# Kernel optimization log

Hardware: AMD Instinct MI355X
Metric: run time of the kernel (lower is better)

Reference implementation:

```python
import jax, jax.numpy as jnp
import numpy as np

# CUBA-LIF constants (from LavaNetwork.__init__ with beta=0.95)
THRESHOLD = 1.0
CURRENT_DECAY = 1.0   # current[t] = (1-1.0)*current[t-1] + input[t] == input[t]
VOLTAGE_DECAY = 1.0 - 0.95  # = 0.05, so v[t] = 0.95*v[t-1] + cur[t]

N_INPUT, N_HIDDEN, N_OUTPUT = 512, 2048, 4 * 64
B, T = 32, 1024


def setup_inputs() -> dict:
    key = jax.random.key(0)
    kx, k1, k2, k3, k4 = jax.random.split(key, 5)
    x = (jax.random.uniform(kx, (B, N_INPUT, T)) < 0.1).astype(jnp.float32)
    # learned params (Linear with bias); small scale so spiking is reasonable
    w1 = jax.random.normal(k1, (N_HIDDEN, N_INPUT), dtype=jnp.float32) * (1.0 / np.sqrt(N_INPUT))
    b1 = jax.random.normal(k2, (N_HIDDEN,), dtype=jnp.float32) * 0.01
    w2 = jax.random.normal(k3, (N_OUTPUT, N_HIDDEN), dtype=jnp.float32) * (1.0 / np.sqrt(N_HIDDEN))
    b2 = jax.random.normal(k4, (N_OUTPUT,), dtype=jnp.float32) * 0.01
    return {"x": x, "w1": w1, "b1": b1, "w2": w2, "b2": b2}


def _cuba_lif(cur):
    """CUBA neuron with current_decay=1 (current==synaptic input),
    leaky-integrate voltage, fire at threshold, reset voltage to 0.
    cur: (B, N, T) -> spikes (B, N, T)."""
    beta_v = 1.0 - VOLTAGE_DECAY  # 0.95

    def step(v, c_t):
        v = v * beta_v + c_t
        s = (v >= THRESHOLD).astype(v.dtype)
        v = v * (1.0 - s)  # reset-to-zero on spike (Loihi behavior)
        return v, s

    cur_t = jnp.moveaxis(cur, -1, 0)  # (T, B, N)
    v0 = jnp.zeros(cur.shape[:-1], cur.dtype)
    _, spk = jax.lax.scan(step, v0, cur_t)
    return jnp.moveaxis(spk, 0, -1)  # (B, N, T)


def reference(x, w1, b1, w2, b2):
    # layer 1: synapse (einsum 'bit,oi->bot' + bias) -> CUBA neuron
    cur1 = jnp.einsum('bit,oi->bot', x, w1) + b1[None, :, None]
    spk1 = _cuba_lif(cur1)
    # layer 2
    cur2 = jnp.einsum('bit,oi->bot', spk1, w2) + b2[None, :, None]
    spk2 = _cuba_lif(cur2)
    return (spk1, spk2)
```

## Files before the change

kernel.cpp:

```cpp
#include <hip/hip_runtime.h>


typedef int i32x4 __attribute__((ext_vector_type(4)));
typedef _Float16 f16x8 __attribute__((ext_vector_type(8)));
typedef _Float16 f16x4 __attribute__((ext_vector_type(4)));
typedef float f32x4 __attribute__((ext_vector_type(4)));

#define GLDS(g, l) __builtin_amdgcn_global_load_lds( \
    (const __attribute__((address_space(1))) void*)(g), \
    (__attribute__((address_space(3))) void*)(l), 16, 0, 0)

#define INV231 4.656612873077392578125e-10


__global__ __launch_bounds__(256) void prep_w8(const float* __restrict__ A,
                                               signed char* __restrict__ wp,
                                               int M, int K)
{
    long gt = (long)blockIdx.x * 256 + threadIdx.x;
    int kq4 = K >> 2;
    int m = (int)(gt / kq4), kq = (int)(gt % kq4);
    int k0 = kq * 4;
    int kt = k0 >> 6, kin = k0 & 63;
    int cw = ((kin >> 4) ^ (m >> 1)) & 3;
    float4 w = *(const float4*)&A[(long)m * K + k0];
    float wv[4] = {w.x, w.y, w.z, w.w};
    int pack[4] = {0, 0, 0, 0};
#pragma unroll
    for (int e = 0; e < 4; e++) {
        long k64 = (long)rint((double)wv[e] * 2147483648.0);
#pragma unroll
        for (int j = 0; j < 3; j++) {
            long r = ((k64 + 128) & 255) - 128;
            pack[j] |= ((int)r & 255) << (e * 8);
            k64 = (k64 - r) >> 8;
        }
        pack[3] |= ((int)k64 & 255) << (e * 8);
    }
#pragma unroll
    for (int p = 0; p < 4; p++)
        *(int*)&wp[(((long)kt * 4 + p) * M + m) * 64 + cw * 16 + (kin & 15)] = pack[p];
}

__global__ __launch_bounds__(256) void prep_x8(const float* __restrict__ x,
                                               unsigned char* __restrict__ xt)
{
    __shared__ float xs[64][68];
    const int b = blockIdx.z, i0 = blockIdx.y * 64, t0 = blockIdx.x * 64;
    const float* xb = x + ((long)b * 512 + i0) * 1024 + t0;
#pragma unroll
    for (int p = 0; p < 4; p++) {
        int f = threadIdx.x + p * 256;
        int i = f >> 4, t4 = (f & 15) * 4;
        *(float4*)&xs[i][t4] = *(const float4*)&xb[(long)i * 1024 + t4];
    }
    __syncthreads();
    int tt = threadIdx.x >> 2, c = threadIdx.x & 3;
    unsigned char bytes[16];
#pragma unroll
    for (int j = 0; j < 16; j++)
        bytes[j] = (unsigned char)xs[c * 16 + j][tt];
    *(uint4*)&xt[(((long)b * 8 + (i0 >> 6)) * 1024 + t0 + tt) * 64 + c * 16] =
        *(uint4*)bytes;
}

__global__ __launch_bounds__(576, 1) void gemm_lif1(
    const signed char* __restrict__ wp,
    const unsigned char* __restrict__ act,
    const float* __restrict__ bias,
    unsigned* __restrict__ mask_ws)
{
    __shared__ signed char Ws[8][4][64][64];
    __shared__ float cs[2][64][64];

    const int m0 = blockIdx.x * 64, b = blockIdx.y;
    const int tid = threadIdx.x, lane = tid & 63, wave = tid >> 6;
    const int lm = lane & 15, lq = lane >> 4;
    const int fro = ((lq ^ (lm >> 1)) & 3) * 16;
    const int mw = wave & 3;
    const int tw2 = wave >> 2;
    const unsigned char* ab = act + (long)b * 8 * 1024 * 64;

    i32x4 areg[4][2];
    double bv = 0.0;

    if (wave < 8) {
        const int gl_row = lane >> 2, gl_col = (lane & 3) * 16;
#pragma unroll
        for (int j = 0; j < 4; ++j) {
            const int r = wave + 8 * j;
            const int kt = r >> 2, pl = r & 3;
            const signed char* g = wp + ((long)r * 2048 + m0 + gl_row) * 64 + gl_col;
#pragma unroll
            for (int q = 0; q < 4; ++q)
                GLDS(g + q * 16 * 64, &Ws[kt][pl][q * 16][0]);
        }
        bv = (double)bias[m0 + mw * 16 + lm];
#pragma unroll
        for (int f = 0; f < 2; f++)
            areg[0][f] = *(const i32x4*)
                &ab[((long)(tw2 * 32 + f * 16 + lm)) * 64 + lq * 16];
#pragma unroll
        for (int f = 0; f < 2; f++)
            areg[1][f] = *(const i32x4*)
                &ab[((long)1 * 1024 + tw2 * 32 + f * 16 + lm) * 64 + lq * 16];
    }
    __syncthreads();

    double u = 0.0;
    bool sprev = false;

    for (int p = 0; p < 17; ++p) {
        if (wave < 8 && p < 16) {
            i32x4 acc[4][2];
#pragma unroll
            for (int pp = 0; pp < 4; pp++)
#pragma unroll
                for (int f = 0; f < 2; f++) acc[pp][f] = (i32x4)0;

#pragma unroll
            for (int kk = 0; kk < 8; ++kk) {
                {
                    int vn = p * 8 + kk + 2;
                    if (vn > 127) vn = 127;
                    const int pn = vn >> 3, kn = vn & 7;
                    const long tt = (long)pn * 64 + tw2 * 32 + lm;
#pragma unroll
                    for (int f = 0; f < 2; f++)
                        areg[(kk + 2) & 3][f] = *(const i32x4*)
                            &ab[((long)kn * 1024 + tt + f * 16) * 64 + lq * 16];
                }
                __builtin_amdgcn_s_setprio(1);
#pragma unroll
                for (int pl = 0; pl < 4; pl++) {
                    i32x4 w0 = *(const i32x4*)&Ws[kk][pl][mw * 16 + lm][fro];
#pragma unroll
                    for (int f = 0; f < 2; f++)
                        acc[pl][f] = __builtin_amdgcn_mfma_i32_16x16x64_i8(
                            areg[kk & 3][f], w0, acc[pl][f], 0, 0, 0);
                }
                __builtin_amdgcn_s_setprio(0);
            }
#pragma unroll
            for (int tf = 0; tf < 2; tf++)
#pragma unroll
                for (int r = 0; r < 4; r++) {
                    long T = acc[3][tf][r];
                    T = T * 256 + acc[2][tf][r];
                    T = T * 256 + acc[1][tf][r];
                    T = T * 256 + acc[0][tf][r];
                    cs[p & 1][tw2 * 32 + tf * 16 + lq * 4 + r][mw * 16 + lm] =
                        (float)((double)T * INV231 + bv);
                }
        }
        if (wave == 8 && p >= 1) {
            const int pq = p - 1, buf = pq & 1;
            float cvA[32], cvB[32];
#pragma unroll
            for (int j = 0; j < 32; ++j) cvA[j] = cs[buf][j][lane];
#pragma unroll
            for (int j = 0; j < 32; ++j) cvB[j] = cs[buf][32 + j][lane];
            {
                unsigned mword = 0;
#pragma unroll
                for (int j = 0; j < 32; ++j) {
                    double c = (double)cvA[j];
                    double a = 0.95 * u + c;
                    u = sprev ? c : a;
                    bool s = (u >= 1.0);
                    mword |= (s ? 1u : 0u) << j;
                    sprev = s;
                }
                mask_ws[((long)b * 32 + pq * 2 + 0) * 2048 + m0 + lane] = mword;
            }
            {
                unsigned mword = 0;
#pragma unroll
                for (int j = 0; j < 32; ++j) {
                    double c = (double)cvB[j];
                    double a = 0.95 * u + c;
                    u = sprev ? c : a;
                    bool s = (u >= 1.0);
                    mword |= (s ? 1u : 0u) << j;
                    sprev = s;
                }
                mask_ws[((long)b * 32 + pq * 2 + 1) * 2048 + m0 + lane] = mword;
            }
        }
        asm volatile("s_waitcnt lgkmcnt(0)" ::: "memory");
        __builtin_amdgcn_s_barrier();
        __builtin_amdgcn_sched_barrier(0);
    }
}

__global__ __launch_bounds__(256) void expand_both(
    const unsigned* __restrict__ mask_ws,
    unsigned char* __restrict__ spk8,
    float* __restrict__ spk1)
{
    __shared__ unsigned msk[64][33];
    const int b = blockIdx.x, kt = blockIdx.y;
    const int tid = threadIdx.x;
#pragma unroll
    for (int i = 0; i < 8; ++i) {
        int idx = tid + i * 256;
        int tw = idx >> 6, m = idx & 63;
        msk[m][tw] = mask_ws[((long)b * 32 + tw) * 2048 + kt * 64 + m];
    }
    __syncthreads();
    unsigned char* dst = spk8 + ((long)b * 32 + kt) * 1024 * 64;
#pragma unroll
    for (int i = 0; i < 16; ++i) {
        int off = tid + i * 256;
        int t = off >> 2, mq = off & 3;
        int tw = t >> 5, sh = t & 31;
        unsigned w0 = 0, w1 = 0, w2 = 0, w3 = 0;
#pragma unroll
        for (int j = 0; j < 4; ++j) {
            w0 |= ((msk[mq * 16 + j][tw] >> sh) & 1u) << (8 * j);
            w1 |= ((msk[mq * 16 + 4 + j][tw] >> sh) & 1u) << (8 * j);
            w2 |= ((msk[mq * 16 + 8 + j][tw] >> sh) & 1u) << (8 * j);
            w3 |= ((msk[mq * 16 + 12 + j][tw] >> sh) & 1u) << (8 * j);
        }
        *(uint4*)&dst[(long)off * 16] = (uint4){w0, w1, w2, w3};
    }
    const int rr = tid >> 5, l5 = tid & 31;
    const int sh1 = (l5 & 7) * 4;
#pragma unroll
    for (int rep = 0; rep < 8; ++rep) {
        const int row = rr + rep * 8;
        float* d1 = spk1 + ((long)b * 2048 + kt * 64 + row) * 1024;
#pragma unroll
        for (int j = 0; j < 8; j++) {
            const int t = l5 * 4 + j * 128;
            const unsigned w = msk[row][(l5 >> 3) + j * 4];
            float4 o;
            o.x = ((w >> sh1) & 1u) ? 1.f : 0.f;
            o.y = ((w >> (sh1 + 1)) & 1u) ? 1.f : 0.f;
            o.z = ((w >> (sh1 + 2)) & 1u) ? 1.f : 0.f;
            o.w = ((w >> (sh1 + 3)) & 1u) ? 1.f : 0.f;
            *(float4*)&d1[t] = o;
        }
    }
}

template <bool TRANS, int NITER, int CHUNK>
__global__ __launch_bounds__(256, 2) void gemm_i8(
    const signed char* __restrict__ wp,
    const unsigned char* __restrict__ act,
    const float* __restrict__ bias,
    float* __restrict__ C,
    int M)
{
    constexpr int NCHUNK = NITER / CHUNK;
    __shared__ signed char Ws[CHUNK][4][32][64];

    const int b = blockIdx.y;
    const int m0 = blockIdx.z * 32, t0 = blockIdx.x * 256;
    const int tid = threadIdx.x, lane = tid & 63, wave = tid >> 6;
    const int wt = t0 + wave * 64;
    const int lm = lane & 15, lq = lane >> 4;
    const int fro = ((lq ^ (lm >> 1)) & 3) * 16;
    const int gl_row = lane >> 2, gl_col = (lane & 3) * 16;

    const unsigned char* ab = act + (long)b * NITER * 1024 * 64;

    auto stage = [&](int cc) {
#pragma unroll
        for (int j = 0; j < CHUNK; ++j) {
            const int r = wave + 4 * j;
            const int kt = r >> 2, p = r & 3;
            const long kg = ((long)(cc * CHUNK + kt) * 4 + p);
            const signed char* g = wp + (kg * M + m0 + gl_row) * 64 + gl_col;
            GLDS(g, &Ws[kt][p][0][0]);
            GLDS(g + 16 * 64, &Ws[kt][p][16][0]);
        }
    };

    i32x4 acc[4][8];
#pragma unroll
    for (int p = 0; p < 4; p++)
#pragma unroll
        for (int q = 0; q < 8; q++) acc[p][q] = (i32x4)0;

    stage(0);
    i32x4 areg[2][4];
#pragma unroll
    for (int f = 0; f < 4; f++)
        areg[0][f] = *(const i32x4*)&ab[((long)(wt + f * 16 + lm)) * 64 + lq * 16];
    __syncthreads();

    for (int c = 0; c < NCHUNK; ++c) {
#pragma unroll
        for (int kk = 0; kk < CHUNK; ++kk) {
            {
                const int itv = c * CHUNK + kk;
                const long nx = (itv + 1 < NITER) ? itv + 1 : itv;
#pragma unroll
                for (int f = 0; f < 4; f++)
                    areg[(kk + 1) & 1][f] = *(const i32x4*)
                        &ab[(nx * 1024 + wt + f * 16 + lm) * 64 + lq * 16];
            }
#pragma unroll
            for (int p = 0; p < 4; p++) {
                i32x4 w0 = *(const i32x4*)&Ws[kk][p][lm][fro];
                i32x4 w1 = *(const i32x4*)&Ws[kk][p][16 + lm][fro];
                if (TRANS) {
#pragma unroll
                    for (int f = 0; f < 4; f++) {
                        acc[p][f * 2 + 0] = __builtin_amdgcn_mfma_i32_16x16x64_i8(
                            areg[kk & 1][f], w0, acc[p][f * 2 + 0], 0, 0, 0);
                        acc[p][f * 2 + 1] = __builtin_amdgcn_mfma_i32_16x16x64_i8(
                            areg[kk & 1][f], w1, acc[p][f * 2 + 1], 0, 0, 0);
                    }
                } else {
#pragma unroll
                    for (int f = 0; f < 4; f++) {
                        acc[p][0 + f] = __builtin_amdgcn_mfma_i32_16x16x64_i8(
                            w0, areg[kk & 1][f], acc[p][0 + f], 0, 0, 0);
                        acc[p][4 + f] = __builtin_amdgcn_mfma_i32_16x16x64_i8(
                            w1, areg[kk & 1][f], acc[p][4 + f], 0, 0, 0);
                    }
                }
            }
        }
        if (c + 1 < NCHUNK) {
            __syncthreads();
            stage(c + 1);
            __syncthreads();
        }
    }

    if (TRANS) {
        double bv[2];
        bv[0] = (double)bias[m0 + lm];
        bv[1] = (double)bias[m0 + 16 + lm];
        float* Cb = C + (long)b * 1024 * M;
#pragma unroll
        for (int tf = 0; tf < 4; tf++)
#pragma unroll
            for (int r = 0; r < 4; r++) {
                const int trow = wt + tf * 16 + lq * 4 + r;
#pragma unroll
                for (int mf = 0; mf < 2; mf++) {
                    long T = acc[3][tf * 2 + mf][r];
                    T = T * 256 + acc[2][tf * 2 + mf][r];
                    T = T * 256 + acc[1][tf * 2 + mf][r];
                    T = T * 256 + acc[0][tf * 2 + mf][r];
                    Cb[(long)trow * M + m0 + mf * 16 + lm] =
                        (float)((double)T * INV231 + bv[mf]);
                }
            }
    } else {
        float* Cb = C + (long)b * M * 1024;
#pragma unroll
        for (int mf = 0; mf < 2; mf++)
#pragma unroll
            for (int r = 0; r < 4; r++) {
                const int mrow = m0 + mf * 16 + lq * 4 + r;
                const double bv = (double)bias[mrow];
#pragma unroll
                for (int tf = 0; tf < 4; tf++) {
                    long T = acc[3][mf * 4 + tf][r];
                    T = T * 256 + acc[2][mf * 4 + tf][r];
                    T = T * 256 + acc[1][mf * 4 + tf][r];
                    T = T * 256 + acc[0][mf * 4 + tf][r];
                    Cb[(long)mrow * 1024 + wt + tf * 16 + lm] =
                        (float)((double)T * INV231 + bv);
                }
            }
    }
}

template <int RPB>
__global__ __launch_bounds__(256) void lif_lds(float* __restrict__ cur)
{
    __shared__ float cs[RPB][36];
    const long rowbase = (long)blockIdx.x * RPB;
    float* base = cur + rowbase * 1024;
    const int tid = threadIdx.x;
    double v = 0.0;
    const int NV = RPB * 32 / 4;
    for (int tc = 0; tc < 1024; tc += 32) {
        for (int f = tid; f < NV; f += 256) {
            int row = f >> 3, t4 = (f & 7) * 4;
            *(float4*)&cs[row][t4] = *(const float4*)&base[(long)row * 1024 + tc + t4];
        }
        __syncthreads();
        if (tid < RPB) {
            float cv[32];
#pragma unroll
            for (int j = 0; j < 32; j++) cv[j] = cs[tid][j];
#pragma unroll
            for (int j = 0; j < 32; j++) {
                v = 0.95 * v + (double)cv[j];
                bool s = v >= 1.0;
                cs[tid][j] = s ? 1.f : 0.f;
                if (s) v = 0.0;
            }
        }
        __syncthreads();
        for (int f = tid; f < NV; f += 256) {
            int row = f >> 3, t4 = (f & 7) * 4;
            *(float4*)&base[(long)row * 1024 + tc + t4] = *(float4*)&cs[row][t4];
        }
        __syncthreads();
    }
}


__device__ inline void split3(float w, _Float16& q0, _Float16& q1, _Float16& q2) {
    float p0 = rintf(w * 4096.f) * 2.44140625e-4f;
    float r1 = w - p0;
    float p1s = rintf(r1 * 8388608.f) * 2.44140625e-4f;
    float r2 = r1 - p1s * 4.8828125e-4f;
    float p2s = rintf(r2 * 1.7179869184e10f) * 1.220703125e-4f;
    q0 = (_Float16)p0; q1 = (_Float16)p1s; q2 = (_Float16)p2s;
}

__global__ __launch_bounds__(256) void gemm_f16x3_kernel(
    const float* __restrict__ A, const float* __restrict__ Bmat,
    const float* __restrict__ bias, float* __restrict__ C,
    int M, int N, int K, long sB, long sC)
{
    __shared__ _Float16 As[3][128][40];
    __shared__ _Float16 Bsh[128][40];
    const int batch = blockIdx.z;
    const float* Bp = Bmat + (long)batch * sB;
    float* Cp = C + (long)batch * sC;
    const int m0 = blockIdx.y * 128, n0 = blockIdx.x * 128;
    const int tid = threadIdx.x, lane = tid & 63, wave = tid >> 6;
    const int wrow = (wave >> 1) * 64, wcol = (wave & 1) * 64;
    const int lm = lane & 15, lq = lane >> 4;
    const int a_mo = tid >> 3, a_kc = (tid & 7) * 4;
    const int b_kq = tid >> 5, b_nq = tid & 31;

    f32x4 acc[3][4][4];
#pragma unroll
    for (int p = 0; p < 3; p++)
#pragma unroll
        for (int i = 0; i < 4; i++)
#pragma unroll
            for (int j = 0; j < 4; j++) acc[p][i][j] = (f32x4)0.f;

    for (int k0 = 0; k0 < K; k0 += 32) {
#pragma unroll
        for (int i = 0; i < 4; i++) {
            const int m = i * 32 + a_mo;
            float4 w = *(const float4*)&A[(long)(m0 + m) * K + k0 + a_kc];
            _Float16 a0[4], a1[4], a2[4];
            split3(w.x, a0[0], a1[0], a2[0]);
            split3(w.y, a0[1], a1[1], a2[1]);
            split3(w.z, a0[2], a1[2], a2[2]);
            split3(w.w, a0[3], a1[3], a2[3]);
            *(f16x4*)&As[0][m][a_kc] = (f16x4){a0[0], a0[1], a0[2], a0[3]};
            *(f16x4*)&As[1][m][a_kc] = (f16x4){a1[0], a1[1], a1[2], a1[3]};
            *(f16x4*)&As[2][m][a_kc] = (f16x4){a2[0], a2[1], a2[2], a2[3]};
        }
        {
            float4 r0 = *(const float4*)&Bp[(long)(k0 + b_kq * 4 + 0) * N + n0 + b_nq * 4];
            float4 r1 = *(const float4*)&Bp[(long)(k0 + b_kq * 4 + 1) * N + n0 + b_nq * 4];
            float4 r2 = *(const float4*)&Bp[(long)(k0 + b_kq * 4 + 2) * N + n0 + b_nq * 4];
            float4 r3 = *(const float4*)&Bp[(long)(k0 + b_kq * 4 + 3) * N + n0 + b_nq * 4];
            *(f16x4*)&Bsh[b_nq * 4 + 0][b_kq * 4] =
                (f16x4){(_Float16)r0.x, (_Float16)r1.x, (_Float16)r2.x, (_Float16)r3.x};
            *(f16x4*)&Bsh[b_nq * 4 + 1][b_kq * 4] =
                (f16x4){(_Float16)r0.y, (_Float16)r1.y, (_Float16)r2.y, (_Float16)r3.y};
            *(f16x4*)&Bsh[b_nq * 4 + 2][b_kq * 4] =
                (f16x4){(_Float16)r0.z, (_Float16)r1.z, (_Float16)r2.z, (_Float16)r3.z};
            *(f16x4*)&Bsh[b_nq * 4 + 3][b_kq * 4] =
                (f16x4){(_Float16)r0.w, (_Float16)r1.w, (_Float16)r2.w, (_Float16)r3.w};
        }
        __syncthreads();
        f16x8 bf[4];
#pragma unroll
        for (int j = 0; j < 4; j++)
            bf[j] = *(const f16x8*)&Bsh[wcol + j * 16 + lm][lq * 8];
#pragma unroll
        for (int p = 0; p < 3; p++) {
            f16x8 af[4];
#pragma unroll
            for (int i = 0; i < 4; i++)
                af[i] = *(const f16x8*)&As[p][wrow + i * 16 + lm][lq * 8];
#pragma unroll
            for (int i = 0; i < 4; i++)
#pragma unroll
                for (int j = 0; j < 4; j++)
                    acc[p][i][j] = __builtin_amdgcn_mfma_f32_16x16x32_f16(
                        af[i], bf[j], acc[p][i][j], 0, 0, 0);
        }
        __syncthreads();
    }
#pragma unroll
    for (int i = 0; i < 4; i++)
#pragma unroll
        for (int r = 0; r < 4; r++) {
            const int row = m0 + wrow + i * 16 + lq * 4 + r;
            const double bv = (double)bias[row];
#pragma unroll
            for (int j = 0; j < 4; j++) {
                double s = (double)acc[0][i][j][r]
                         + (double)acc[1][i][j][r] * 4.8828125e-4
                         + (double)acc[2][i][j][r] * 4.76837158203125e-7 + bv;
                Cp[(long)row * N + n0 + wcol + j * 16 + lm] = (float)s;
            }
        }
}

__global__ __launch_bounds__(256) void lif_rows(float* __restrict__ data,
                                                long nrows, int T)
{
    long r = (long)blockIdx.x * blockDim.x + threadIdx.x;
    if (r >= nrows) return;
    float* p = data + r * (long)T;
    double v = 0.0;
    for (int t = 0; t < T; t += 4) {
        float4 c = *(float4*)(p + t);
        float4 s;
        v = 0.95 * v + (double)c.x; s.x = (v >= 1.0) ? 1.f : 0.f; if (v >= 1.0) v = 0.0;
        v = 0.95 * v + (double)c.y; s.y = (v >= 1.0) ? 1.f : 0.f; if (v >= 1.0) v = 0.0;
        v = 0.95 * v + (double)c.z; s.z = (v >= 1.0) ? 1.f : 0.f; if (v >= 1.0) v = 0.0;
        v = 0.95 * v + (double)c.w; s.w = (v >= 1.0) ? 1.f : 0.f; if (v >= 1.0) v = 0.0;
        *(float4*)(p + t) = s;
    }
}


extern "C" void kernel_launch(void* const* d_in, const int* in_sizes, int n_in,
                              void* d_out, int out_size, void* d_ws, size_t ws_size,
                              hipStream_t stream)
{
    const float* x  = (const float*)d_in[0];
    const float* w1 = (const float*)d_in[1];
    const float* b1 = (const float*)d_in[2];
    const float* w2 = (const float*)d_in[3];
    const float* b2 = (const float*)d_in[4];

    float* out  = (float*)d_out;
    float* spk1 = out;
    float* spk2 = out + (long)32 * 2048 * 1024;

    const size_t WP1 = 4194304;
    const size_t WP2 = 2097152;
    const size_t X8T = 16777216;
    const size_t SPK = 67108864;
    const size_t MSK = 8388608;
    const size_t NEED = WP1 + WP2 + X8T + SPK + MSK;

    if (ws_size >= NEED) {
        char* ws = (char*)d_ws;
        signed char* wp1 = (signed char*)ws;
        signed char* wp2 = (signed char*)(ws + WP1);
        unsigned char* x8t = (unsigned char*)(ws + WP1 + WP2);
        unsigned char* spk8 = (unsigned char*)(ws + WP1 + WP2 + X8T);
        unsigned* mask_ws = (unsigned*)(ws + WP1 + WP2 + X8T + SPK);

        prep_w8<<<1024, 256, 0, stream>>>(w1, wp1, 2048, 512);
        prep_w8<<<512, 256, 0, stream>>>(w2, wp2, 256, 2048);
        prep_x8<<<dim3(16, 8, 32), 256, 0, stream>>>(x, x8t);

        gemm_lif1<<<dim3(32, 32), 576, 0, stream>>>(wp1, x8t, b1, mask_ws);

        expand_both<<<dim3(32, 32), 256, 0, stream>>>(mask_ws, spk8, spk1);

        gemm_i8<false, 32, 8><<<dim3(4, 32, 8), 256, 0, stream>>>(
            wp2, spk8, b2, spk2, 256);
        lif_lds<32><<<256, 256, 0, stream>>>(spk2);
    } else {
        gemm_f16x3_kernel<<<dim3(8, 16, 32), 256, 0, stream>>>(
            w1, x, b1, spk1, 2048, 1024, 512, (long)512 * 1024, (long)2048 * 1024);
        lif_rows<<<(65536 + 255) / 256, 256, 0, stream>>>(spk1, 65536, 1024);
        gemm_f16x3_kernel<<<dim3(8, 2, 32), 256, 0, stream>>>(
            w2, spk1, b2, spk2, 256, 1024, 2048, (long)2048 * 1024, (long)256 * 1024);
        lif_rows<<<(8192 + 255) / 256, 256, 0, stream>>>(spk2, 8192, 1024);
    }
}
```

Baseline: 630.3 us.

## Fuse layer-2 int8 GEMM with LIF scan using producer/consumer waves

Replaces the separate layer-2 int8 GEMM and LDS-based LIF kernel with one kernel. Four waves compute 128-timestep tiles of currents into a double-buffered LDS tile while a fifth wave runs the sequential LIF recurrence on the previous tile and writes spikes directly. This removes the float current round trip through global memory and one kernel launch. In exchange, grid parallelism drops to 512 blocks of 16 rows each at one block per CU, and the serial LIF wave may become the bottleneck.

```diff
diff --git a/kernel.cpp b/kernel.cpp
--- a/kernel.cpp
+++ b/kernel.cpp
@@ -244,167 +244,157 @@
     }
 }
 
-template <bool TRANS, int NITER, int CHUNK>
-__global__ __launch_bounds__(256, 2) void gemm_i8(
+__global__ __launch_bounds__(320, 1) void gemm_lif2(
     const signed char* __restrict__ wp,
     const unsigned char* __restrict__ act,
     const float* __restrict__ bias,
-    float* __restrict__ C,
-    int M)
-{
-    constexpr int NCHUNK = NITER / CHUNK;
-    __shared__ signed char Ws[CHUNK][4][32][64];
-
-    const int b = blockIdx.y;
-    const int m0 = blockIdx.z * 32, t0 = blockIdx.x * 256;
+    float* __restrict__ spk2)
+{
+    __shared__ signed char Ws[32][4][16][64];
+    __shared__ float cs[2][128][17];
+
+    const int b = blockIdx.x, m0 = blockIdx.y * 16;
     const int tid = threadIdx.x, lane = tid & 63, wave = tid >> 6;
-    const int wt = t0 + wave * 64;
     const int lm = lane & 15, lq = lane >> 4;
     const int fro = ((lq ^ (lm >> 1)) & 3) * 16;
-    const int gl_row = lane >> 2, gl_col = (lane & 3) * 16;
-
-    const unsigned char* ab = act + (long)b * NITER * 1024 * 64;
-
-    auto stage = [&](int cc) {
-#pragma unroll
-        for (int j = 0; j < CHUNK; ++j) {
+    const unsigned char* ab = act + (long)b * 32 * 1024 * 64;
+
+    i32x4 areg[4][2];
+    double bvr[4] = {0.0, 0.0, 0.0, 0.0};
+
+    if (wave < 4) {
+        const int gl_row = lane >> 2, gl_col = (lane & 3) * 16;
+#pragma unroll
+        for (int j = 0; j < 32; ++j) {
             const int r = wave + 4 * j;
-            const int kt = r >> 2, p = r & 3;
-            const long kg = ((long)(cc * CHUNK + kt) * 4 + p);
-            const signed char* g = wp + (kg * M + m0 + gl_row) * 64 + gl_col;
-            GLDS(g, &Ws[kt][p][0][0]);
-            GLDS(g + 16 * 64, &Ws[kt][p][16][0]);
-        }
-    };
-
-    i32x4 acc[4][8];
-#pragma unroll
-    for (int p = 0; p < 4; p++)
-#pragma unroll
-        for (int q = 0; q < 8; q++) acc[p][q] = (i32x4)0;
-
-    stage(0);
-    i32x4 areg[2][4];
-#pragma unroll
-    for (int f = 0; f < 4; f++)
-        areg[0][f] = *(const i32x4*)&ab[((long)(wt + f * 16 + lm)) * 64 + lq * 16];
+            const int kt = r >> 2, pl = r & 3;
+            const signed char* g =
+                wp + (((long)kt * 4 + pl) * 256 + m0 + gl_row) * 64 + gl_col;
+            GLDS(g, &Ws[kt][pl][0][0]);
+        }
+#pragma unroll
+        for (int r = 0; r < 4; ++r)
+            bvr[r] = (double)bias[m0 + lq * 4 + r];
+        {
+            const long wt0 = wave * 32 + lm;
+#pragma unroll
+            for (int f = 0; f < 2; f++)
+                areg[0][f] = *(const i32x4*)&ab[(wt0 + f * 16) * 64 + lq * 16];
+#pragma unroll
+            for (int f = 0; f < 2; f++)
+                areg[1][f] = *(const i32x4*)
+                    &ab[((long)1 * 1024 + wt0 + f * 16) * 64 + lq * 16];
+        }
+    }
     __syncthreads();
 
-    for (int c = 0; c < NCHUNK; ++c) {
-#pragma unroll
-        for (int kk = 0; kk < CHUNK; ++kk) {
+    double u = 0.0;
+    bool sprev = false;
+    float* sp2 = spk2 + ((long)b * 256 + m0 + (lane & 15)) * 1024;
+
+    for (int p = 0; p < 9; ++p) {
+        if (wave < 4 && p < 8) {
+            i32x4 acc[4][2];
+#pragma unroll
+            for (int pp = 0; pp < 4; pp++)
+#pragma unroll
+                for (int f = 0; f < 2; f++) acc[pp][f] = (i32x4)0;
+
+#pragma unroll 4
+            for (int kt = 0; kt < 32; ++kt) {
+                {
+                    int vn = p * 32 + kt + 2;
+                    if (vn > 255) vn = 255;
+                    const int pn = vn >> 5, kn = vn & 31;
+                    const long tt = (long)pn * 128 + wave * 32 + lm;
+#pragma unroll
+                    for (int f = 0; f < 2; f++)
+                        areg[(kt + 2) & 3][f] = *(const i32x4*)
+                            &ab[((long)kn * 1024 + tt + f * 16) * 64 + lq * 16];
+                }
+                __builtin_amdgcn_s_setprio(1);
+#pragma unroll
+                for (int pl = 0; pl < 4; pl++) {
+                    i32x4 w0 = *(const i32x4*)&Ws[kt][pl][lm][fro];
+#pragma unroll
+                    for (int f = 0; f < 2; f++)
+                        acc[pl][f] = __builtin_amdgcn_mfma_i32_16x16x64_i8(
+                            w0, areg[kt & 3][f], acc[pl][f], 0, 0, 0);
+                }
+                __builtin_amdgcn_s_setprio(0);
+            }
+#pragma unroll
+            for (int tf = 0; tf < 2; tf++)
+#pragma unroll
+                for (int r = 0; r < 4; r++) {
+                    long T = acc[3][tf][r];
+                    T = T * 256 + acc[2][tf][r];
+                    T = T * 256 + acc[1][tf][r];
+                    T = T * 256 + acc[0][tf][r];
+                    cs[p & 1][wave * 32 + tf * 16 + lm][lq * 4 + r] =
+                        (float)((double)T * INV231 + bvr[r]);
+                }
+        }
+        if (wave == 4 && p >= 1 && lane < 16) {
+            const int pq = p - 1, buf = pq & 1;
+            float* sp = sp2 + pq * 128;
+            float cvA[32], cvB[32];
+#pragma unroll
+            for (int j = 0; j < 32; ++j) cvA[j] = cs[buf][j][lane];
+#pragma unroll
+            for (int j = 0; j < 32; ++j) cvB[j] = cs[buf][32 + j][lane];
             {
-                const int itv = c * CHUNK + kk;
-                const long nx = (itv + 1 < NITER) ? itv + 1 : itv;
-#pragma unroll
-                for (int f = 0; f < 4; f++)
-                    areg[(kk + 1) & 1][f] = *(const i32x4*)
-                        &ab[(nx * 1024 + wt + f * 16 + lm) * 64 + lq * 16];
-            }
-#pragma unroll
-            for (int p = 0; p < 4; p++) {
-                i32x4 w0 = *(const i32x4*)&Ws[kk][p][lm][fro];
-                i32x4 w1 = *(const i32x4*)&Ws[kk][p][16 + lm][fro];
-                if (TRANS) {
-#pragma unroll
-                    for (int f = 0; f < 4; f++) {
-                        acc[p][f * 2 + 0] = __builtin_amdgcn_mfma_i32_16x16x64_i8(
-                            areg[kk & 1][f], w0, acc[p][f * 2 + 0], 0, 0, 0);
-                        acc[p][f * 2 + 1] = __builtin_amdgcn_mfma_i32_16x16x64_i8(
-                            areg[kk & 1][f], w1, acc[p][f * 2 + 1], 0, 0, 0);
-                    }
-                } else {
-#pragma unroll
-                    for (int f = 0; f < 4; f++) {
-                        acc[p][0 + f] = __builtin_amdgcn_mfma_i32_16x16x64_i8(
-                            w0, areg[kk & 1][f], acc[p][0 + f], 0, 0, 0);
-                        acc[p][4 + f] = __builtin_amdgcn_mfma_i32_16x16x64_i8(
-                            w1, areg[kk & 1][f], acc[p][4 + f], 0, 0, 0);
-                    }
-                }
-            }
-        }
-        if (c + 1 < NCHUNK) {
-            __syncthreads();
-            stage(c + 1);
-            __syncthreads();
-        }
-    }
-
-    if (TRANS) {
-        double bv[2];
-        bv[0] = (double)bias[m0 + lm];
-        bv[1] = (double)bias[m0 + 16 + lm];
-        float* Cb = C + (long)b * 1024 * M;
-#pragma unroll
-        for (int tf = 0; tf < 4; tf++)
-#pragma unroll
-            for (int r = 0; r < 4; r++) {
-                const int trow = wt + tf * 16 + lq * 4 + r;
-#pragma unroll
-                for (int mf = 0; mf < 2; mf++) {
-                    long T = acc[3][tf * 2 + mf][r];
-                    T = T * 256 + acc[2][tf * 2 + mf][r];
-                    T = T * 256 + acc[1][tf * 2 + mf][r];
-                    T = T * 256 + acc[0][tf * 2 + mf][r];
-                    Cb[(long)trow * M + m0 + mf * 16 + lm] =
-                        (float)((double)T * INV231 + bv[mf]);
-                }
-            }
-    } else {
-        float* Cb = C + (long)b * M * 1024;
-#pragma unroll
-        for (int mf = 0; mf < 2; mf++)
-#pragma unroll
-            for (int r = 0; r < 4; r++) {
-                const int mrow = m0 + mf * 16 + lq * 4 + r;
-                const double bv = (double)bias[mrow];
-#pragma unroll
-                for (int tf = 0; tf < 4; tf++) {
-                    long T = acc[3][mf * 4 + tf][r];
-                    T = T * 256 + acc[2][mf * 4 + tf][r];
-                    T = T * 256 + acc[1][mf * 4 + tf][r];
-                    T = T * 256 + acc[0][mf * 4 + tf][r];
-                    Cb[(long)mrow * 1024 + wt + tf * 16 + lm] =
-                        (float)((double)T * INV231 + bv);
-                }
-            }
-    }
-}
-
-template <int RPB>
-__global__ __launch_bounds__(256) void lif_lds(float* __restrict__ cur)
-{
-    __shared__ float cs[RPB][36];
-    const long rowbase = (long)blockIdx.x * RPB;
-    float* base = cur + rowbase * 1024;
-    const int tid = threadIdx.x;
-    double v = 0.0;
-    const int NV = RPB * 32 / 4;
-    for (int tc = 0; tc < 1024; tc += 32) {
-        for (int f = tid; f < NV; f += 256) {
-            int row = f >> 3, t4 = (f & 7) * 4;
-            *(float4*)&cs[row][t4] = *(const float4*)&base[(long)row * 1024 + tc + t4];
-        }
-        __syncthreads();
-        if (tid < RPB) {
-            float cv[32];
-#pragma unroll
-            for (int j = 0; j < 32; j++) cv[j] = cs[tid][j];
-#pragma unroll
-            for (int j = 0; j < 32; j++) {
-                v = 0.95 * v + (double)cv[j];
-                bool s = v >= 1.0;
-                cs[tid][j] = s ? 1.f : 0.f;
-                if (s) v = 0.0;
-            }
-        }
-        __syncthreads();
-        for (int f = tid; f < NV; f += 256) {
-            int row = f >> 3, t4 = (f & 7) * 4;
-            *(float4*)&base[(long)row * 1024 + tc + t4] = *(float4*)&cs[row][t4];
-        }
-        __syncthreads();
+#pragma unroll
+                for (int j = 0; j < 32; ++j) {
+                    double c = (double)cvA[j];
+                    double a = 0.95 * u + c;
+                    u = sprev ? c : a;
+                    bool s = (u >= 1.0);
+                    sp[j] = s ? 1.f : 0.f;
+                    sprev = s;
+                }
+            }
+#pragma unroll
+            for (int j = 0; j < 32; ++j) cvA[j] = cs[buf][64 + j][lane];
+            {
+#pragma unroll
+                for (int j = 0; j < 32; ++j) {
+                    double c = (double)cvB[j];
+                    double a = 0.95 * u + c;
+                    u = sprev ? c : a;
+                    bool s = (u >= 1.0);
+                    sp[32 + j] = s ? 1.f : 0.f;
+                    sprev = s;
+                }
+            }
+#pragma unroll
+            for (int j = 0; j < 32; ++j) cvB[j] = cs[buf][96 + j][lane];
+            {
+#pragma unroll
+                for (int j = 0; j < 32; ++j) {
+                    double c = (double)cvA[j];
+                    double a = 0.95 * u + c;
+                    u = sprev ? c : a;
+                    bool s = (u >= 1.0);
+                    sp[64 + j] = s ? 1.f : 0.f;
+                    sprev = s;
+                }
+            }
+            {
+#pragma unroll
+                for (int j = 0; j < 32; ++j) {
+                    double c = (double)cvB[j];
+                    double a = 0.95 * u + c;
+                    u = sprev ? c : a;
+                    bool s = (u >= 1.0);
+                    sp[96 + j] = s ? 1.f : 0.f;
+                    sprev = s;
+                }
+            }
+        }
+        asm volatile("s_waitcnt lgkmcnt(0)" ::: "memory");
+        __builtin_amdgcn_s_barrier();
+        __builtin_amdgcn_sched_barrier(0);
     }
 }
 
@@ -563,9 +553,7 @@
 
         expand_both<<<dim3(32, 32), 256, 0, stream>>>(mask_ws, spk8, spk1);
 
-        gemm_i8<false, 32, 8><<<dim3(4, 32, 8), 256, 0, stream>>>(
-            wp2, spk8, b2, spk2, 256);
-        lif_lds<32><<<256, 256, 0, stream>>>(spk2);
+        gemm_lif2<<<dim3(32, 16), 320, 0, stream>>>(wp2, spk8, b2, spk2);
     } else {
         gemm_f16x3_kernel<<<dim3(8, 16, 32), 256, 0, stream>>>(
             w1, x, b1, spk1, 2048, 1024, 512, (long)512 * 1024, (long)2048 * 1024);
```

Result: slower. 644.6 us (+2.3%).
